# Kernel tuning notes

Hardware: AMD Instinct MI355X
Metric: run time of the kernel (lower is better)

Reference implementation:

```python
import jax, jax.numpy as jnp
import numpy as np

N = 100000      # nodes
E = 1600000     # edges (before self-loops)
IN_DIM = 128
HID = 32
HEADS = 4
EMB = 128
SLOPE = 0.2     # PyG GATConv default negative_slope


def setup_inputs() -> dict:
    key = jax.random.key(0)
    ks = jax.random.split(key, 16)
    def glorot(k, shape):
        fan_in = shape[0] if len(shape) > 1 else shape[-1]
        return jax.random.normal(k, shape, jnp.float32) * (1.0 / np.sqrt(fan_in))
    x = jax.random.normal(ks[0], (N, IN_DIM), jnp.float32)
    edge_index = jax.random.randint(ks[1], (2, E), 0, N)
    return {
        "x": x,
        "edge_index": edge_index,
        # layer 1: in_dim -> hidden (heads=4, concat)
        "W1": glorot(ks[2], (IN_DIM, HEADS * HID)),
        "att_src1": glorot(ks[3], (HEADS, HID)),
        "att_dst1": glorot(ks[4], (HEADS, HID)),
        "b1": jnp.zeros((HEADS * HID,), jnp.float32),
        # layer 2: hidden*heads -> hidden (heads=4, concat)
        "W2": glorot(ks[5], (HEADS * HID, HEADS * HID)),
        "att_src2": glorot(ks[6], (HEADS, HID)),
        "att_dst2": glorot(ks[7], (HEADS, HID)),
        "b2": jnp.zeros((HEADS * HID,), jnp.float32),
        # layer 3: hidden*heads -> embed (heads=1)
        "W3": glorot(ks[8], (HEADS * HID, EMB)),
        "att_src3": glorot(ks[9], (1, EMB)),
        "att_dst3": glorot(ks[10], (1, EMB)),
        "b3": jnp.zeros((EMB,), jnp.float32),
    }


def gat_conv(x, src, dst, W, att_src, att_dst, b, heads, out_ch):
    """One PyG-style GATConv (concat=True). src/dst already include self-loops."""
    n = x.shape[0]
    h = (x @ W).reshape(n, heads, out_ch)                 # [N,H,C]
    a_s = jnp.einsum('nhc,hc->nh', h, att_src)            # [N,H]
    a_d = jnp.einsum('nhc,hc->nh', h, att_dst)            # [N,H]
    e = jax.nn.leaky_relu(a_s[src] + a_d[dst], SLOPE)     # [E',H]
    # numerically stable softmax over irregular incoming neighborhoods (per dst)
    m = jax.ops.segment_max(e, dst, num_segments=n)       # [N,H]
    ex = jnp.exp(e - m[dst])
    denom = jax.ops.segment_sum(ex, dst, num_segments=n)  # [N,H]
    alpha = ex / denom[dst]                                # [E',H]
    out = jax.ops.segment_sum(h[src] * alpha[:, :, None], dst, num_segments=n)
    return out.reshape(n, heads * out_ch) + b


def reference(x, edge_index, W1, att_src1, att_dst1, b1,
              W2, att_src2, att_dst2, b2, W3, att_src3, att_dst3, b3):
    n = x.shape[0]
    loops = jnp.arange(n, dtype=edge_index.dtype)
    src = jnp.concatenate([edge_index[0], loops])  # PyG add_self_loops=True
    dst = jnp.concatenate([edge_index[1], loops])
    h = gat_conv(x, src, dst, W1, att_src1, att_dst1, b1, HEADS, HID)
    h = jax.nn.elu(h)
    h = gat_conv(h, src, dst, W2, att_src2, att_dst2, b2, HEADS, HID)
    h = jax.nn.elu(h)
    out = gat_conv(h, src, dst, W3, att_src3, att_dst3, b3, 1, EMB)
    return out
```

## Files before the change

### kernel.cpp

```cpp
#include <hip/hip_runtime.h>
#include <hip/hip_fp16.h>
#include <math.h>

#define N_NODES 100000
#define N_EDGES 1600000
#define SLOPE 0.2f

#define BSHIFT 8
#define NB 391
#define CHUNK 8192

typedef _Float16 f16x8 __attribute__((ext_vector_type(8)));
typedef float f32x4 __attribute__((ext_vector_type(4)));
typedef float f32x8v __attribute__((ext_vector_type(8)));

__global__ __launch_bounds__(256) void partA1(const int* __restrict__ ei,
                                              int* __restrict__ bucket_count,
                                              int* __restrict__ blkcnt,
                                              int E, int n, int nblk) {
  __shared__ int cnt[NB];
  for (int i = threadIdx.x; i < NB; i += 256) cnt[i] = 0;
  __syncthreads();
  int b = blockIdx.x;
  int base = b * CHUNK;
  int total = E + n;
  int lim = min(base + CHUNK, total);
  for (int e = base + threadIdx.x; e < lim; e += 256) {
    int d = (e < E) ? ei[E + e] : (e - E);
    atomicAdd(&cnt[d >> BSHIFT], 1);
  }
  __syncthreads();
  for (int i = threadIdx.x; i < NB; i += 256) {
    int c = cnt[i];
    blkcnt[i * nblk + b] = c;
    if (c) atomicAdd(&bucket_count[i], c);
  }
}

__global__ __launch_bounds__(512) void scan_nb(
    const int* __restrict__ bucket_count, int* __restrict__ bucket_base) {
  __shared__ int lds[512];
  int t = threadIdx.x;
  int v = (t < NB) ? bucket_count[t] : 0;
  int x = v;
  lds[t] = x;
  __syncthreads();
  for (int off = 1; off < 512; off <<= 1) {
    int y = (t >= off) ? lds[t - off] : 0;
    __syncthreads();
    x += y;
    lds[t] = x;
    __syncthreads();
  }
  int excl = x - v;
  if (t <= NB) bucket_base[t] = excl;
}

__global__ __launch_bounds__(256) void scan_blk(
    const int* __restrict__ blkcnt, const int* __restrict__ bucket_base,
    int* __restrict__ blk_base, int nblk) {
  __shared__ int lds[256];
  int i = blockIdx.x;
  int t = threadIdx.x;
  int v = (t < nblk) ? blkcnt[i * nblk + t] : 0;
  int x = v;
  lds[t] = x;
  __syncthreads();
  for (int off = 1; off < 256; off <<= 1) {
    int y = (t >= off) ? lds[t - off] : 0;
    __syncthreads();
    x += y;
    lds[t] = x;
    __syncthreads();
  }
  if (t < nblk) blk_base[i * nblk + t] = bucket_base[i] + (x - v);
}

__global__ __launch_bounds__(256) void partA2(const int* __restrict__ ei,
                                              const int* __restrict__ blk_base,
                                              unsigned* __restrict__ part,
                                              int E, int n, int nblk) {
  __shared__ int res[NB];
  int b = blockIdx.x;
  for (int i = threadIdx.x; i < NB; i += 256) res[i] = blk_base[i * nblk + b];
  __syncthreads();
  int base = b * CHUNK;
  int total = E + n;
  int lim = min(base + CHUNK, total);
  for (int e = base + threadIdx.x; e < lim; e += 256) {
    int s, d;
    if (e < E) { s = ei[e]; d = ei[E + e]; } else { s = d = e - E; }
    int bk = d >> BSHIFT;
    int pos = atomicAdd(&res[bk], 1);
    part[pos] = ((unsigned)s << BSHIFT) | (unsigned)(d & 255);
  }
}

__global__ __launch_bounds__(256) void passB(const unsigned* __restrict__ part,
                                             const int* __restrict__ bucket_base,
                                             int* __restrict__ row_start,
                                             int* __restrict__ edge_src, int n) {
  __shared__ int cnt[256];
  __shared__ int sc[256];
  __shared__ int loff[256];
  int b = blockIdx.x;
  int t = threadIdx.x;
  int node0 = b << BSHIFT;
  int bstart = bucket_base[b], bend = bucket_base[b + 1];
  cnt[t] = 0;
  __syncthreads();
  for (int i = bstart + t; i < bend; i += 256)
    atomicAdd(&cnt[part[i] & 255], 1);
  __syncthreads();
  int v = cnt[t];
  int x = v;
  sc[t] = x;
  __syncthreads();
  for (int off = 1; off < 256; off <<= 1) {
    int y = (t >= off) ? sc[t - off] : 0;
    __syncthreads();
    x += y;
    sc[t] = x;
    __syncthreads();
  }
  int excl = x - v;
  loff[t] = excl;
  int node = node0 + t;
  if (node < n) row_start[node] = bstart + excl;
  if (b == NB - 1 && t == 0) row_start[n] = bucket_base[NB];
  __syncthreads();
  for (int i = bstart + t; i < bend; i += 256) {
    unsigned p = part[i];
    int dl = p & 255;
    int pos = bstart + atomicAdd(&loff[dl], 1);
    edge_src[pos] = (int)(p >> BSHIFT);
  }
}

__global__ __launch_bounds__(256) void convert_w(
    const float* __restrict__ W1, const float* __restrict__ W2,
    const float* __restrict__ W3, __half* __restrict__ Wt1,
    __half* __restrict__ Wt2, __half* __restrict__ Wt3) {
  int idx = blockIdx.x * 256 + threadIdx.x;
  if (idx >= 3 * 16384) return;
  int mat = idx >> 14;
  int r = idx & 16383;
  int k = r >> 7, col = r & 127;
  const float* W = (mat == 0) ? W1 : (mat == 1) ? W2 : W3;
  __half* Wt = (mat == 0) ? Wt1 : (mat == 1) ? Wt2 : Wt3;
  Wt[col * 128 + k] = __float2half(W[k * 128 + col]);
}

template <int H, typename InT>
__global__ __launch_bounds__(256, 4) void gemm_att_mfma(
    const InT* __restrict__ X, const __half* __restrict__ Wt,
    const float* __restrict__ att_src, const float* __restrict__ att_dst,
    __half* __restrict__ Y, float* __restrict__ a_s, float* __restrict__ a_d,
    int n) {
  __shared__ _Float16 B_lds[128 * 128];
  int t = threadIdx.x;
  int r0 = blockIdx.x * 64;
  int wv = t >> 6, lane = t & 63, quad = lane >> 4, l15 = lane & 15;

  {
    const __half* wp = Wt + t * 64;
    int brow = t >> 1;
    int sbase = (t & 1) * 8;
#pragma unroll
    for (int i = 0; i < 8; i++) {
      int slot = (sbase + i) ^ (brow & 15);
      *(float4*)&B_lds[brow * 128 + slot * 8] = *(const float4*)(wp + i * 8);
    }
  }

  int arow = r0 + wv * 16 + l15;
  bool inb = arow < n;
  f16x8 a[4];
  if constexpr (sizeof(InT) == 4) {
    const float* xp = (const float*)X + (size_t)arow * 128 + quad * 8;
#pragma unroll
    for (int kb = 0; kb < 4; kb++) {
      float4 v0, v1;
      if (inb) {
        v0 = *(const float4*)(xp + kb * 32);
        v1 = *(const float4*)(xp + kb * 32 + 4);
      } else {
        v0 = make_float4(0.f, 0.f, 0.f, 0.f);
        v1 = v0;
      }
      f32x8v f = {v0.x, v0.y, v0.z, v0.w, v1.x, v1.y, v1.z, v1.w};
      a[kb] = __builtin_convertvector(f, f16x8);
    }
  } else {
    const __half* xp = (const __half*)X + (size_t)arow * 128 + quad * 8;
    f16x8 z = {};
#pragma unroll
    for (int kb = 0; kb < 4; kb++) {
      if (inb) a[kb] = *(const f16x8*)(xp + kb * 32);
      else a[kb] = z;
    }
  }
  __syncthreads();

  f32x4 acc[8];
#pragma unroll
  for (int ct = 0; ct < 8; ct++) acc[ct] = (f32x4){0.f, 0.f, 0.f, 0.f};

#pragma unroll
  for (int kb = 0; kb < 4; kb++) {
#pragma unroll
    for (int ct = 0; ct < 8; ct++) {
      f16x8 b = *(const f16x8*)(
          &B_lds[(ct * 16 + l15) * 128 + (((kb * 4 + quad) ^ l15) * 8)]);
      acc[ct] = __builtin_amdgcn_mfma_f32_16x16x32_f16(a[kb], b, acc[ct], 0, 0, 0);
    }
  }

  int rbase = r0 + wv * 16 + quad * 4;

  float avs[8], avd[8];
#pragma unroll
  for (int ct = 0; ct < 8; ct++) {
    avs[ct] = att_src[ct * 16 + l15];
    avd[ct] = att_dst[ct * 16 + l15];
  }
  if constexpr (H == 4) {
    float ps[4][4], pd_[4][4];
#pragma unroll
    for (int hd = 0; hd < 4; hd++)
#pragma unroll
      for (int reg = 0; reg < 4; reg++) { ps[hd][reg] = 0.f; pd_[hd][reg] = 0.f; }
#pragma unroll
    for (int ct = 0; ct < 8; ct++) {
      int hd = ct >> 1;
#pragma unroll
      for (int reg = 0; reg < 4; reg++) {
        ps[hd][reg] = fmaf(acc[ct][reg], avs[ct], ps[hd][reg]);
        pd_[hd][reg] = fmaf(acc[ct][reg], avd[ct], pd_[hd][reg]);
      }
    }
#pragma unroll
    for (int off = 1; off <= 8; off <<= 1)
#pragma unroll
      for (int hd = 0; hd < 4; hd++)
#pragma unroll
        for (int reg = 0; reg < 4; reg++) {
          ps[hd][reg] += __shfl_xor(ps[hd][reg], off, 64);
          pd_[hd][reg] += __shfl_xor(pd_[hd][reg], off, 64);
        }
#pragma unroll
    for (int hd = 0; hd < 4; hd++)
      if (l15 == hd) {
#pragma unroll
        for (int reg = 0; reg < 4; reg++) {
          int row = rbase + reg;
          if (row < n) {
            a_s[row * 4 + hd] = ps[hd][reg];
            a_d[row * 4 + hd] = pd_[hd][reg];
          }
        }
      }
  } else {
    float ps[4] = {}, pd_[4] = {};
#pragma unroll
    for (int ct = 0; ct < 8; ct++)
#pragma unroll
      for (int reg = 0; reg < 4; reg++) {
        ps[reg] = fmaf(acc[ct][reg], avs[ct], ps[reg]);
        pd_[reg] = fmaf(acc[ct][reg], avd[ct], pd_[reg]);
      }
#pragma unroll
    for (int off = 1; off <= 8; off <<= 1)
#pragma unroll
      for (int reg = 0; reg < 4; reg++) {
        ps[reg] += __shfl_xor(ps[reg], off, 64);
        pd_[reg] += __shfl_xor(pd_[reg], off, 64);
      }
    if (l15 == 0) {
#pragma unroll
      for (int reg = 0; reg < 4; reg++) {
        int row = rbase + reg;
        if (row < n) { a_s[row] = ps[reg]; a_d[row] = pd_[reg]; }
      }
    }
  }

  __syncthreads();
  {
    const int LW = 136;
    _Float16* wreg = &B_lds[wv * 16 * LW];
#pragma unroll
    for (int reg = 0; reg < 4; reg++) {
      int rl = quad * 4 + reg;
#pragma unroll
      for (int ct = 0; ct < 8; ct++)
        wreg[rl * LW + ct * 16 + l15] = (_Float16)acc[ct][reg];
    }
#pragma unroll
    for (int j = 0; j < 4; j++) {
      int rl = j * 4 + (lane >> 4);
      int seg = lane & 15;
      int rowg = r0 + wv * 16 + rl;
      if (rowg < n) {
        float4 v = *(const float4*)&wreg[rl * LW + seg * 8];
        *(float4*)(Y + (size_t)rowg * 128 + seg * 8) = v;
      }
    }
  }
}

template <int H, bool DO_ELU, typename OutT>
__global__ __launch_bounds__(256) void agg_kernel(
    const __half* __restrict__ h, const float* __restrict__ a_s,
    const float* __restrict__ a_d, const int* __restrict__ row_start,
    const int* __restrict__ edge_src, const float* __restrict__ bias,
    OutT* __restrict__ out, int n) {
  const int C = 128 / H;
  __shared__ float w_lds[4][H * 66];
  __shared__ int sn_lds[4][64];
  int wslot = threadIdx.x >> 6;
  int wid = (blockIdx.x * blockDim.x + threadIdx.x) >> 6;
  int lane = threadIdx.x & 63;
  if (wid >= n) return;
  int start = row_start[wid], end = row_start[wid + 1];
  int deg = end - start;

  float adv[H];
#pragma unroll
  for (int hh = 0; hh < H; hh++) adv[hh] = a_d[wid * H + hh];

  if (deg <= 64) {
    bool valid = lane < deg;
    int sn = valid ? edge_src[start + lane] : 0;
    float e[H];
    if (valid) {
      if constexpr (H == 4) {
        float4 asv = *(const float4*)(a_s + (size_t)sn * 4);
        float t0 = asv.x + adv[0];
        float t1 = asv.y + adv[1];
        float t2 = asv.z + adv[2];
        float t3 = asv.w + adv[3];
        e[0] = t0 >= 0.f ? t0 : SLOPE * t0;
        e[1] = t1 >= 0.f ? t1 : SLOPE * t1;
        e[2] = t2 >= 0.f ? t2 : SLOPE * t2;
        e[3] = t3 >= 0.f ? t3 : SLOPE * t3;
      } else {
        float tt = a_s[sn] + adv[0];
        e[0] = tt >= 0.f ? tt : SLOPE * tt;
      }
    } else {
#pragma unroll
      for (int hh = 0; hh < H; hh++) e[hh] = -1e30f;
    }
    bool small = (deg <= 32);
    float w[H], s[H];
#pragma unroll
    for (int hh = 0; hh < H; hh++) {
      w[hh] = valid ? __expf(e[hh] - 40.f) : 0.f;
      s[hh] = w[hh];
    }
#pragma unroll
    for (int off = 1; off <= 16; off <<= 1)
#pragma unroll
      for (int hh = 0; hh < H; hh++) s[hh] += __shfl_xor(s[hh], off, 64);
    if (!small)
#pragma unroll
      for (int hh = 0; hh < H; hh++) s[hh] += __shfl_xor(s[hh], 32, 64);
    sn_lds[wslot][lane] = sn << 8;
#pragma unroll
    for (int hh = 0; hh < H; hh++)
      w_lds[wslot][hh * 66 + lane] = valid ? w[hh] * (1.f / s[hh]) : 0.f;
    __builtin_amdgcn_wave_barrier();

    int g = lane >> 4, l = lane & 15;
    int d0 = l * 8;
    const char* hb = (const char*)h + l * 16;
    int headBase = (H == 4) ? (l >> 2) * 66 : 0;
    f32x8v acc = {};
    int degp16 = (deg + 15) & ~15;
    for (int eidx = 0; eidx < degp16; eidx += 16) {
#pragma unroll
      for (int jj = 0; jj < 4; jj++) {
        int ei2 = eidx + jj * 4 + g;
        int boff = sn_lds[wslot][ei2];
        float wv = w_lds[wslot][headBase + ei2];
        f16x8 hv = *(const f16x8*)(hb + (unsigned)boff);
        f32x8v pf = __builtin_convertvector(hv, f32x8v);
        f32x8v ws = {wv, wv, wv, wv, wv, wv, wv, wv};
        acc = pf * ws + acc;
      }
    }
    float o[8];
#pragma unroll
    for (int k = 0; k < 8; k++) {
      float v = acc[k];
      v += __shfl_xor(v, 16, 64);
      v += __shfl_xor(v, 32, 64);
      o[k] = v;
    }
    if (lane < 16) {
      float4 bv0 = *(const float4*)(bias + d0);
      float4 bv1 = *(const float4*)(bias + d0 + 4);
      o[0] += bv0.x; o[1] += bv0.y; o[2] += bv0.z; o[3] += bv0.w;
      o[4] += bv1.x; o[5] += bv1.y; o[6] += bv1.z; o[7] += bv1.w;
      if (DO_ELU) {
#pragma unroll
        for (int k = 0; k < 8; k++)
          o[k] = (o[k] > 0.f) ? o[k] : __expf(o[k]) - 1.f;
      }
      if constexpr (sizeof(OutT) == 2) {
        union { float4 f4; __half2 h2[4]; } uo;
        uo.h2[0] = __floats2half2_rn(o[0], o[1]);
        uo.h2[1] = __floats2half2_rn(o[2], o[3]);
        uo.h2[2] = __floats2half2_rn(o[4], o[5]);
        uo.h2[3] = __floats2half2_rn(o[6], o[7]);
        *(float4*)((__half*)out + (size_t)wid * 128 + d0) = uo.f4;
      } else {
        float4 ov0 = {o[0], o[1], o[2], o[3]};
        float4 ov1 = {o[4], o[5], o[6], o[7]};
        *(float4*)((float*)out + (size_t)wid * 128 + d0) = ov0;
        *(float4*)((float*)out + (size_t)wid * 128 + d0 + 4) = ov1;
      }
    }
    return;
  }

  {
    const int G = C / 2;
    int head = lane / G;
    float m[H], s[H];
#pragma unroll
    for (int hh = 0; hh < H; hh++) { m[hh] = -1e30f; s[hh] = 0.f; }
    for (int idx = start + lane; idx < end; idx += 64) {
      int sn = edge_src[idx];
#pragma unroll
      for (int hh = 0; hh < H; hh++) {
        float e = a_s[sn * H + hh] + adv[hh];
        e = (e >= 0.f) ? e : SLOPE * e;
        float mn = fmaxf(m[hh], e);
        s[hh] = s[hh] * __expf(m[hh] - mn) + __expf(e - mn);
        m[hh] = mn;
      }
    }
    for (int off = 1; off < 64; off <<= 1) {
#pragma unroll
      for (int hh = 0; hh < H; hh++) {
        float mo = __shfl_xor(m[hh], off, 64);
        float so = __shfl_xor(s[hh], off, 64);
        float mn = fmaxf(m[hh], mo);
        s[hh] = s[hh] * __expf(m[hh] - mn) + so * __expf(mo - mn);
        m[hh] = mn;
      }
    }
    int d0 = lane * 2;
    float mh = m[head];
    float rsh = 1.f / s[head];
    float adh = adv[head];
    float acc0 = 0.f, acc1 = 0.f;
    for (int idx = start; idx < end; idx++) {
      int sn = edge_src[idx];
      float e = a_s[sn * H + head] + adh;
      e = (e >= 0.f) ? e : SLOPE * e;
      float w = __expf(e - mh) * rsh;
      float2 hv = __half22float2(*(const __half2*)(h + (size_t)sn * 128 + d0));
      acc0 += w * hv.x;
      acc1 += w * hv.y;
    }
    float o0 = acc0 + bias[d0];
    float o1 = acc1 + bias[d0 + 1];
    if (DO_ELU) {
      o0 = (o0 > 0.f) ? o0 : __expf(o0) - 1.f;
      o1 = (o1 > 0.f) ? o1 : __expf(o1) - 1.f;
    }
    out[(size_t)wid * 128 + d0] = (OutT)o0;
    out[(size_t)wid * 128 + d0 + 1] = (OutT)o1;
  }
}

extern "C" void kernel_launch(void* const* d_in, const int* in_sizes, int n_in,
                              void* d_out, int out_size, void* d_ws,
                              size_t ws_size, hipStream_t stream) {
  const float* x = (const float*)d_in[0];
  const int* ei = (const int*)d_in[1];
  const float* W1 = (const float*)d_in[2];
  const float* as1 = (const float*)d_in[3];
  const float* ad1 = (const float*)d_in[4];
  const float* b1 = (const float*)d_in[5];
  const float* W2 = (const float*)d_in[6];
  const float* as2 = (const float*)d_in[7];
  const float* ad2 = (const float*)d_in[8];
  const float* b2 = (const float*)d_in[9];
  const float* W3 = (const float*)d_in[10];
  const float* as3 = (const float*)d_in[11];
  const float* ad3 = (const float*)d_in[12];
  const float* b3 = (const float*)d_in[13];
  float* out = (float*)d_out;

  const int n = N_NODES, E = N_EDGES, total = E + n;
  const int nblkA = (total + CHUNK - 1) / CHUNK;

  char* ws = (char*)d_ws;
  size_t off = 0;
  auto alloc = [&](size_t bytes) -> char* {
    char* p = ws + off;
    off = (off + bytes + 255) & ~(size_t)255;
    return p;
  };
  __half* hbuf = (__half*)alloc(sizeof(__half) * (size_t)n * 128);
  float* a_s = (float*)alloc(sizeof(float) * n * 4);
  float* a_d = (float*)alloc(sizeof(float) * n * 4);
  unsigned* part = (unsigned*)alloc(sizeof(unsigned) * total);
  int* edge_src = (int*)alloc(sizeof(int) * total);
  int* row_start = (int*)alloc(sizeof(int) * (n + 1));
  int* bucket_count = (int*)alloc(sizeof(int) * (NB + 1));
  int* bucket_base = (int*)alloc(sizeof(int) * (NB + 1));
  int* blkcnt = (int*)alloc(sizeof(int) * NB * nblkA);
  int* blk_base = (int*)alloc(sizeof(int) * NB * nblkA);
  __half* Wt1 = (__half*)alloc(sizeof(__half) * 16384);
  __half* Wt2 = (__half*)alloc(sizeof(__half) * 16384);
  __half* Wt3 = (__half*)alloc(sizeof(__half) * 16384);
  __half* hbuf2 = (__half*)alloc(sizeof(__half) * (size_t)n * 128);
  bool fp16mid = (off <= ws_size);

  hipMemsetAsync(bucket_count, 0, sizeof(int) * (NB + 1), stream);

  convert_w<<<192, 256, 0, stream>>>(W1, W2, W3, Wt1, Wt2, Wt3);

  partA1<<<nblkA, 256, 0, stream>>>(ei, bucket_count, blkcnt, E, n, nblkA);
  scan_nb<<<1, 512, 0, stream>>>(bucket_count, bucket_base);
  scan_blk<<<NB, 256, 0, stream>>>(blkcnt, bucket_base, blk_base, nblkA);
  partA2<<<nblkA, 256, 0, stream>>>(ei, blk_base, part, E, n, nblkA);
  passB<<<NB, 256, 0, stream>>>(part, bucket_base, row_start, edge_src, n);

  int agg_blocks = (n + 3) / 4;
  int gemm_blocks = (n + 63) / 64;

  if (fp16mid) {
    gemm_att_mfma<4, float><<<gemm_blocks, 256, 0, stream>>>(
        x, Wt1, as1, ad1, hbuf, a_s, a_d, n);
    agg_kernel<4, true, __half><<<agg_blocks, 256, 0, stream>>>(
        hbuf, a_s, a_d, row_start, edge_src, b1, hbuf2, n);

    gemm_att_mfma<4, __half><<<gemm_blocks, 256, 0, stream>>>(
        hbuf2, Wt2, as2, ad2, hbuf, a_s, a_d, n);
    agg_kernel<4, true, __half><<<agg_blocks, 256, 0, stream>>>(
        hbuf, a_s, a_d, row_start, edge_src, b2, hbuf2, n);

    gemm_att_mfma<1, __half><<<gemm_blocks, 256, 0, stream>>>(
        hbuf2, Wt3, as3, ad3, hbuf, a_s, a_d, n);
    agg_kernel<1, false, float><<<agg_blocks, 256, 0, stream>>>(
        hbuf, a_s, a_d, row_start, edge_src, b3, out, n);
  } else {
    gemm_att_mfma<4, float><<<gemm_blocks, 256, 0, stream>>>(
        x, Wt1, as1, ad1, hbuf, a_s, a_d, n);
    agg_kernel<4, true, float><<<agg_blocks, 256, 0, stream>>>(
        hbuf, a_s, a_d, row_start, edge_src, b1, out, n);

    gemm_att_mfma<4, float><<<gemm_blocks, 256, 0, stream>>>(
        out, Wt2, as2, ad2, hbuf, a_s, a_d, n);
    agg_kernel<4, true, float><<<agg_blocks, 256, 0, stream>>>(
        hbuf, a_s, a_d, row_start, edge_src, b2, out, n);

    gemm_att_mfma<1, float><<<gemm_blocks, 256, 0, stream>>>(
        out, Wt3, as3, ad3, hbuf, a_s, a_d, n);
    agg_kernel<1, false, float><<<agg_blocks, 256, 0, stream>>>(
        hbuf, a_s, a_d, row_start, edge_src, b3, out, n);
  }
}
```

Measured before the change: 457.1 us.

## Fold bucket memset into weight conversion, pre-swizzle weights, shrink aggregation unroll

Removes the separate memset by zeroing bucket counts inside the convert_w kernel. It also applies the LDS XOR swizzle when the transposed weights are written, so the GEMM can copy them to shared memory linearly. In aggregation, the division becomes a hardware reciprocal, and the edge loop pads to 8 instead of 16 with scalar FMAs, cutting wasted padded work for low-degree nodes. Trade-offs: less memory-level parallelism per iteration and a slightly less accurate reciprocal.

```diff
diff --git a/kernel.cpp b/kernel.cpp
--- a/kernel.cpp
+++ b/kernel.cpp
@@ -140,7 +140,11 @@
 __global__ __launch_bounds__(256) void convert_w(
     const float* __restrict__ W1, const float* __restrict__ W2,
     const float* __restrict__ W3, __half* __restrict__ Wt1,
-    __half* __restrict__ Wt2, __half* __restrict__ Wt3) {
+    __half* __restrict__ Wt2, __half* __restrict__ Wt3,
+    int* __restrict__ bucket_count) {
+  if (blockIdx.x == 0) {
+    for (int i = threadIdx.x; i <= NB; i += 256) bucket_count[i] = 0;
+  }
   int idx = blockIdx.x * 256 + threadIdx.x;
   if (idx >= 3 * 16384) return;
   int mat = idx >> 14;
@@ -148,7 +152,8 @@
   int k = r >> 7, col = r & 127;
   const float* W = (mat == 0) ? W1 : (mat == 1) ? W2 : W3;
   __half* Wt = (mat == 0) ? Wt1 : (mat == 1) ? Wt2 : Wt3;
-  Wt[col * 128 + k] = __float2half(W[k * 128 + col]);
+  int sw = (((k >> 3) ^ (col & 15)) << 3) | (k & 7);
+  Wt[col * 128 + sw] = __float2half(W[k * 128 + col]);
 }
 
 template <int H, typename InT>
@@ -164,13 +169,9 @@
 
   {
     const __half* wp = Wt + t * 64;
-    int brow = t >> 1;
-    int sbase = (t & 1) * 8;
-#pragma unroll
-    for (int i = 0; i < 8; i++) {
-      int slot = (sbase + i) ^ (brow & 15);
-      *(float4*)&B_lds[brow * 128 + slot * 8] = *(const float4*)(wp + i * 8);
-    }
+#pragma unroll
+    for (int i = 0; i < 8; i++)
+      *(float4*)&B_lds[t * 64 + i * 8] = *(const float4*)(wp + i * 8);
   }
 
   int arow = r0 + wv * 16 + l15;
@@ -369,25 +370,26 @@
     sn_lds[wslot][lane] = sn << 8;
 #pragma unroll
     for (int hh = 0; hh < H; hh++)
-      w_lds[wslot][hh * 66 + lane] = valid ? w[hh] * (1.f / s[hh]) : 0.f;
+      w_lds[wslot][hh * 66 + lane] =
+          valid ? w[hh] * __builtin_amdgcn_rcpf(s[hh]) : 0.f;
     __builtin_amdgcn_wave_barrier();
 
     int g = lane >> 4, l = lane & 15;
     int d0 = l * 8;
     const char* hb = (const char*)h + l * 16;
     int headBase = (H == 4) ? (l >> 2) * 66 : 0;
-    f32x8v acc = {};
-    int degp16 = (deg + 15) & ~15;
-    for (int eidx = 0; eidx < degp16; eidx += 16) {
-#pragma unroll
-      for (int jj = 0; jj < 4; jj++) {
+    float acc[8] = {};
+    int degp8 = (deg + 7) & ~7;
+    for (int eidx = 0; eidx < degp8; eidx += 8) {
+#pragma unroll
+      for (int jj = 0; jj < 2; jj++) {
         int ei2 = eidx + jj * 4 + g;
         int boff = sn_lds[wslot][ei2];
         float wv = w_lds[wslot][headBase + ei2];
         f16x8 hv = *(const f16x8*)(hb + (unsigned)boff);
-        f32x8v pf = __builtin_convertvector(hv, f32x8v);
-        f32x8v ws = {wv, wv, wv, wv, wv, wv, wv, wv};
-        acc = pf * ws + acc;
+#pragma unroll
+        for (int k = 0; k < 8; k++)
+          acc[k] = fmaf((float)hv[k], wv, acc[k]);
       }
     }
     float o[8];
@@ -522,9 +524,7 @@
   __half* hbuf2 = (__half*)alloc(sizeof(__half) * (size_t)n * 128);
   bool fp16mid = (off <= ws_size);
 
-  hipMemsetAsync(bucket_count, 0, sizeof(int) * (NB + 1), stream);
-
-  convert_w<<<192, 256, 0, stream>>>(W1, W2, W3, Wt1, Wt2, Wt3);
+  convert_w<<<192, 256, 0, stream>>>(W1, W2, W3, Wt1, Wt2, Wt3, bucket_count);
 
   partA1<<<nblkA, 256, 0, stream>>>(ei, bucket_count, blkcnt, E, n, nblkA);
   scan_nb<<<1, 512, 0, stream>>>(bucket_count, bucket_base);
```

Result: no change. 457.0 us (-0.0%).
